# Kernel optimization log

Hardware: AMD Instinct MI355X
Metric: run time of the kernel (lower is better)

The kernel has to match this reference:

```python
import jax, jax.numpy as jnp
import numpy as np

N_NODES = 100000
N_EDGES = 3200000
F_IN = 256
H = 256
L = 256
BN_EPS = 1e-5


def gcn_conv(x, src, dst, deg_inv_sqrt, W, b):
    # x: [N, Fin]; src/dst: [E+N] (self-loops appended); returns [N, Fout]
    h = x @ W  # dense transform first (Fout may be < Fin)
    norm = deg_inv_sqrt[src] * deg_inv_sqrt[dst]  # [E+N]
    msg = h[src] * norm[:, None]                  # gather
    out = jax.ops.segment_sum(msg, dst, num_segments=N_NODES)  # scatter-add
    return out + b


def batch_norm(x, gamma, beta):
    # BatchNorm1d in training mode: per-feature mean/var over the node dim
    mean = jnp.mean(x, axis=0)
    var = jnp.var(x, axis=0)
    return (x - mean) * jax.lax.rsqrt(var + BN_EPS) * gamma + beta


def setup_inputs() -> dict:
    key = jax.random.key(0)
    ks = jax.random.split(key, 8)
    x = jax.random.normal(ks[0], (N_NODES, F_IN), dtype=jnp.float32)
    edge_index = jax.random.randint(ks[1], (2, N_EDGES), 0, N_NODES, dtype=jnp.int64)
    # glorot-ish init for weights
    W1 = jax.random.normal(ks[2], (F_IN, H), dtype=jnp.float32) * (1.0 / np.sqrt(F_IN))
    b1 = jnp.zeros((H,), dtype=jnp.float32)
    W_mu = jax.random.normal(ks[3], (H, L), dtype=jnp.float32) * (1.0 / np.sqrt(H))
    b_mu = jnp.zeros((L,), dtype=jnp.float32)
    W_ls = jax.random.normal(ks[4], (H, L), dtype=jnp.float32) * (1.0 / np.sqrt(H))
    b_ls = jnp.zeros((L,), dtype=jnp.float32)
    gamma = jnp.ones((H,), dtype=jnp.float32)
    beta = jnp.zeros((H,), dtype=jnp.float32)
    return {"x": x, "edge_index": edge_index, "W1": W1, "b1": b1,
            "W_mu": W_mu, "b_mu": b_mu, "W_ls": W_ls, "b_ls": b_ls,
            "gamma": gamma, "beta": beta}


def reference(x, edge_index, W1, b1, W_mu, b_mu, W_ls, b_ls, gamma, beta):
    # Add self-loops once (shared across the three GCNConv layers)
    loop = jnp.arange(N_NODES, dtype=edge_index.dtype)
    src = jnp.concatenate([edge_index[0], loop])
    dst = jnp.concatenate([edge_index[1], loop])
    deg = jax.ops.segment_sum(jnp.ones_like(dst, dtype=jnp.float32), dst,
                              num_segments=N_NODES)
    deg_inv_sqrt = jnp.where(deg > 0, jax.lax.rsqrt(jnp.maximum(deg, 1.0)), 0.0)

    h = gcn_conv(x, src, dst, deg_inv_sqrt, W1, b1)
    h = jax.nn.relu(batch_norm(h, gamma, beta))
    mu = gcn_conv(h, src, dst, deg_inv_sqrt, W_mu, b_mu)
    logstd = gcn_conv(h, src, dst, deg_inv_sqrt, W_ls, b_ls)
    return (mu, logstd)
```

## Files before the change

kernel.cpp:

```cpp
#include <hip/hip_runtime.h>
#include <hip/hip_bf16.h>

#define FEAT 256
#define NPB 512
#define NPB_SHIFT 9
#define MAXBINS 256
#define CAP 20480
#define BIN_CHUNK 8192

typedef __attribute__((ext_vector_type(8))) short bf16x8;
typedef __attribute__((ext_vector_type(8))) ushort u16x8;
typedef __attribute__((ext_vector_type(4))) float f32x4;

__device__ __forceinline__ float bf2f(ushort h) {
    union { unsigned u; float f; } v; v.u = ((unsigned)h) << 16; return v.f;
}
__device__ __forceinline__ ushort f2bf(float f) {
    union { float f; unsigned u; } v; v.f = f;
    unsigned u = v.u;
    return (ushort)((u + 0x7FFFu + ((u >> 16) & 1u)) >> 16);
}


__global__ __launch_bounds__(256) void k_bin(const int* __restrict__ ei, int E, int N,
                                             int* __restrict__ bincur,
                                             int2* __restrict__ binbuf, int nbins) {
    __shared__ int hist[MAXBINS];
    __shared__ int base[MAXBINS];
    int t = threadIdx.x;
    int T = E + N;
    int start = blockIdx.x * BIN_CHUNK;
    int end = min(start + BIN_CHUNK, T);
    for (int b = t; b < nbins; b += 256) hist[b] = 0;
    __syncthreads();
    for (int idx = start + t; idx < end; idx += 256) {
        int d = (idx < E) ? ei[E + idx] : idx - E;
        atomicAdd(&hist[d >> NPB_SHIFT], 1);
    }
    __syncthreads();
    for (int b = t; b < nbins; b += 256) {
        int c = hist[b];
        base[b] = c ? (b * CAP + atomicAdd(&bincur[b], c)) : 0;
        hist[b] = 0;
    }
    __syncthreads();
    for (int idx = start + t; idx < end; idx += 256) {
        int s, d;
        if (idx < E) { s = ei[idx]; d = ei[E + idx]; }
        else         { s = idx - E; d = idx - E; }
        int b = d >> NPB_SHIFT;
        int local = atomicAdd(&hist[b], 1);
        binbuf[base[b] + local] = make_int2(s, d);
    }
}


__global__ __launch_bounds__(512) void k_histcsr(const int2* __restrict__ binbuf,
                                                 const int* __restrict__ bincur,
                                                 int* __restrict__ offs,
                                                 float* __restrict__ dis,
                                                 int* __restrict__ csr, int N, int nbins) {
    __shared__ int bsh[256];
    __shared__ int h[NPB];
    __shared__ int cur[NPB];
    int b = blockIdx.x;
    int t = threadIdx.x;
    int node0 = b * NPB;
    int nn = min(NPB, N - node0);
    if (t < 256) bsh[t] = (t < nbins) ? bincur[t] : 0;
    h[t] = 0; cur[t] = 0;
    __syncthreads();
    for (int d = 1; d < 256; d <<= 1) {
        int x = (t < 256 && t >= d) ? bsh[t - d] : 0;
        __syncthreads();
        if (t < 256) bsh[t] += x;
        __syncthreads();
    }
    int cnt = bincur[b];
    int bpre = bsh[b] - cnt;
    if (b == 0 && t == 0) offs[N] = bsh[nbins - 1];
    int base = b * CAP;
    for (int i = t; i < cnt; i += 512) {
        atomicAdd(&h[binbuf[base + i].y - node0], 1);
    }
    __syncthreads();
    int v = h[t];
    for (int d = 1; d < 512; d <<= 1) {
        int x = (t >= d) ? h[t - d] : 0;
        __syncthreads();
        h[t] += x;
        __syncthreads();
    }
    int myoff = bpre + h[t] - v;
    if (t < nn) {
        offs[node0 + t] = myoff;
        dis[node0 + t] = rsqrtf((float)v);
    }
    h[t] = myoff;
    __syncthreads();
    for (int i = t; i < cnt; i += 512) {
        int2 e = binbuf[base + i];
        int ld = e.y - node0;
        int c = atomicAdd(&cur[ld], 1);
        csr[h[ld] + c] = e.x;
    }
}


__global__ __launch_bounds__(256) void k_cvt(const float* __restrict__ x,
                                             ushort* __restrict__ y,
                                             const float* __restrict__ dis, int n4) {
    int i = blockIdx.x * blockDim.x + threadIdx.x;
    int stride = gridDim.x * blockDim.x;
    for (; i < n4; i += stride) {
        float d = dis[i >> 6];
        float4 v = ((const float4*)x)[i];
        ushort4 o;
        o.x = f2bf(v.x * d); o.y = f2bf(v.y * d);
        o.z = f2bf(v.z * d); o.w = f2bf(v.w * d);
        ((ushort4*)y)[i] = o;
    }
}


__global__ void k_wprep(const float* __restrict__ W1, const float* __restrict__ Wmu,
                        const float* __restrict__ Wls, const float* __restrict__ bmu,
                        const float* __restrict__ bls,
                        ushort* __restrict__ Wt1, ushort* __restrict__ Wtc,
                        float* __restrict__ biasc, float* __restrict__ bnacc) {
    int i = blockIdx.x * 256 + threadIdx.x;
    int m = i >> 16;
    int j = i & 65535;
    int n = j >> 8, k = j & 255;
    const float* W = (m == 0) ? W1 : (m == 1) ? Wmu : Wls;
    ushort v = f2bf(W[k * 256 + n]);
    if (m == 0) Wt1[j] = v;
    else if (m == 1) Wtc[j] = v;
    else Wtc[65536 + j] = v;
    if (i < 512) { biasc[i] = (i < 256) ? bmu[i] : bls[i - 256]; bnacc[i] = 0.f; }
}


__global__ __launch_bounds__(256) void k_agg(const ushort* __restrict__ in,
                                             ushort* __restrict__ out,
                                             const int* __restrict__ offs,
                                             const int* __restrict__ csr,
                                             const float* __restrict__ dis, int N) {
    int wid = blockIdx.x * 4 + ((int)threadIdx.x >> 6);
    if (wid >= N) return;
    int lane = threadIdx.x & 63;
    int half = lane >> 5;
    int l32 = lane & 31;
    int beg = offs[wid], end = offs[wid + 1];
    float acc[8] = {};
    int k = beg;
    for (; k + 16 <= end; k += 16) {
        int s0 = csr[k + half];
        int s1 = csr[k + 2 + half];
        int s2 = csr[k + 4 + half];
        int s3 = csr[k + 6 + half];
        int s4 = csr[k + 8 + half];
        int s5 = csr[k + 10 + half];
        int s6 = csr[k + 12 + half];
        int s7 = csr[k + 14 + half];
        bf16x8 v0 = *(const bf16x8*)(in + (size_t)s0 * FEAT + l32 * 8);
        bf16x8 v1 = *(const bf16x8*)(in + (size_t)s1 * FEAT + l32 * 8);
        bf16x8 v2 = *(const bf16x8*)(in + (size_t)s2 * FEAT + l32 * 8);
        bf16x8 v3 = *(const bf16x8*)(in + (size_t)s3 * FEAT + l32 * 8);
        bf16x8 v4 = *(const bf16x8*)(in + (size_t)s4 * FEAT + l32 * 8);
        bf16x8 v5 = *(const bf16x8*)(in + (size_t)s5 * FEAT + l32 * 8);
        bf16x8 v6 = *(const bf16x8*)(in + (size_t)s6 * FEAT + l32 * 8);
        bf16x8 v7 = *(const bf16x8*)(in + (size_t)s7 * FEAT + l32 * 8);
        #pragma unroll
        for (int j = 0; j < 8; ++j) {
            float t0 = bf2f((ushort)v0[j]) + bf2f((ushort)v1[j]);
            float t1 = bf2f((ushort)v2[j]) + bf2f((ushort)v3[j]);
            float t2 = bf2f((ushort)v4[j]) + bf2f((ushort)v5[j]);
            float t3 = bf2f((ushort)v6[j]) + bf2f((ushort)v7[j]);
            acc[j] += (t0 + t1) + (t2 + t3);
        }
    }
    for (; k + 2 <= end; k += 2) {
        int s = csr[k + half];
        bf16x8 v = *(const bf16x8*)(in + (size_t)s * FEAT + l32 * 8);
        #pragma unroll
        for (int j = 0; j < 8; ++j) acc[j] += bf2f((ushort)v[j]);
    }
    if (k < end && half == 0) {
        int s = csr[k];
        bf16x8 v = *(const bf16x8*)(in + (size_t)s * FEAT + l32 * 8);
        #pragma unroll
        for (int j = 0; j < 8; ++j) acc[j] += bf2f((ushort)v[j]);
    }
    #pragma unroll
    for (int j = 0; j < 8; ++j) acc[j] += __shfl_xor(acc[j], 32, 64);
    if (half == 0) {
        float d = dis[wid];
        u16x8 o;
        #pragma unroll
        for (int j = 0; j < 8; ++j) o[j] = f2bf(acc[j] * d);
        *(u16x8*)(out + (size_t)wid * FEAT + l32 * 8) = o;
    }
}


template <int NCOL, bool BF16OUT>
__global__ __launch_bounds__(256) void k_gemm(const ushort* __restrict__ A,
                                              const ushort* __restrict__ Bt,
                                              const float* __restrict__ bias,
                                              float* __restrict__ C0,
                                              float* __restrict__ C1,
                                              ushort* __restrict__ Cb,
                                              float* __restrict__ bnacc,
                                              int M, int split) {
    __shared__ ushort At[128 * 256];
    __shared__ ushort Bs[128 * 64];
    int t = threadIdx.x;
    int lane = t & 63;
    int wave = t >> 6;
    int wr = wave >> 1, wc = wave & 1;
    int by = blockIdx.x;
    int lo = lane & 15, g = lane >> 4;

    #pragma unroll
    for (int i = 0; i < 16; ++i) {
        int idx = t + i * 256;
        int r = idx >> 5;
        int c = idx & 31;
        int gr = by * 128 + r;
        bf16x8 av = {};
        if (gr < M) av = *(const bf16x8*)(A + (size_t)gr * 256 + c * 8);
        int pc = (c & 24) | ((c & 7) ^ (r & 7));
        *(bf16x8*)(At + r * 256 + pc * 8) = av;
    }
    __syncthreads();

    constexpr int NH = NCOL / 128;
    for (int nh = 0; nh < NH; ++nh) {
        f32x4 acc[4][4] = {};
        for (int kt = 0; kt < 4; ++kt) {
            #pragma unroll
            for (int u = 0; u < 4; ++u) {
                int idx = t + u * 256;
                int r = idx >> 3, c = idx & 7;
                int lc = c ^ (r & 7);
                bf16x8 bv = *(const bf16x8*)(Bt + (size_t)(nh * 128 + r) * 256 + kt * 64 + lc * 8);
                *(bf16x8*)(Bs + r * 64 + c * 8) = bv;
            }
            __syncthreads();
            #pragma unroll
            for (int h = 0; h < 2; ++h) {
                bf16x8 af[4], bfr[4];
                #pragma unroll
                for (int m = 0; m < 4; ++m) {
                    int r = wr * 64 + m * 16 + lo;
                    af[m] = *(const bf16x8*)(At + r * 256 + (kt * 8 + ((h * 4 + g) ^ (r & 7))) * 8);
                }
                #pragma unroll
                for (int n = 0; n < 4; ++n) {
                    int r = wc * 64 + n * 16 + lo;
                    bfr[n] = *(const bf16x8*)(Bs + r * 64 + ((h * 4 + g) ^ (r & 7)) * 8);
                }
                #pragma unroll
                for (int m = 0; m < 4; ++m)
                    #pragma unroll
                    for (int n = 0; n < 4; ++n)
                        acc[m][n] = __builtin_amdgcn_mfma_f32_16x16x32_bf16(
                            af[m], bfr[n], acc[m][n], 0, 0, 0);
            }
            __syncthreads();
        }
        #pragma unroll
        for (int n = 0; n < 4; ++n) {
            int gc = nh * 128 + wc * 64 + n * 16 + lo;
            float bb = bias[gc];
            float s = 0.f, q = 0.f;
            #pragma unroll
            for (int m = 0; m < 4; ++m) {
                f32x4 v = acc[m][n];
                #pragma unroll
                for (int r4 = 0; r4 < 4; ++r4) {
                    int grow = by * 128 + wr * 64 + m * 16 + g * 4 + r4;
                    if (grow < M) {
                        float val = v[r4] + bb;
                        if (BF16OUT) {
                            Cb[(size_t)grow * 256 + gc] = f2bf(val);
                            s += val; q += val * val;
                        } else {
                            float* Cp = C0; int cc = gc;
                            if (gc >= split) { Cp = C1; cc = gc - split; }
                            __builtin_nontemporal_store(val, &Cp[(size_t)grow * 256 + cc]);
                        }
                    }
                }
            }
            if (BF16OUT) {
                s += __shfl_xor(s, 16, 64); s += __shfl_xor(s, 32, 64);
                q += __shfl_xor(q, 16, 64); q += __shfl_xor(q, 32, 64);
                if (g == 0) {
                    atomicAdd(&bnacc[gc], s);
                    atomicAdd(&bnacc[256 + gc], q);
                }
            }
        }
    }
}


__global__ __launch_bounds__(256) void k_bnapply(const ushort* __restrict__ h,
                                                 ushort* __restrict__ o,
                                                 const float* __restrict__ acc,
                                                 const float* __restrict__ gamma,
                                                 const float* __restrict__ beta,
                                                 const float* __restrict__ dis, int Nn) {
    int c4 = (threadIdx.x & 63) * 4;
    int rof = (int)threadIdx.x >> 6;
    float inv = 1.0f / (float)Nn;
    float g[4], b[4];
    #pragma unroll
    for (int j = 0; j < 4; ++j) {
        float mean = acc[c4 + j] * inv;
        float var = acc[FEAT + c4 + j] * inv - mean * mean;
        float rs = rsqrtf(var + 1e-5f);
        g[j] = gamma[c4 + j] * rs;
        b[j] = beta[c4 + j] - mean * g[j];
    }
    for (int r = blockIdx.x * 4 + rof; r < Nn; r += gridDim.x * 4) {
        float d = dis[r];
        ushort4 v = *(const ushort4*)(h + (size_t)r * FEAT + c4);
        float o0 = bf2f(v.x) * g[0] + b[0], o1 = bf2f(v.y) * g[1] + b[1];
        float o2 = bf2f(v.z) * g[2] + b[2], o3 = bf2f(v.w) * g[3] + b[3];
        ushort4 ov;
        ov.x = f2bf((o0 > 0.f ? o0 : 0.f) * d);
        ov.y = f2bf((o1 > 0.f ? o1 : 0.f) * d);
        ov.z = f2bf((o2 > 0.f ? o2 : 0.f) * d);
        ov.w = f2bf((o3 > 0.f ? o3 : 0.f) * d);
        *(ushort4*)(o + (size_t)r * FEAT + c4) = ov;
    }
}


extern "C" void kernel_launch(void* const* d_in, const int* in_sizes, int n_in,
                              void* d_out, int out_size, void* d_ws, size_t ws_size,
                              hipStream_t stream) {
    const float* x     = (const float*)d_in[0];
    const int*   ei    = (const int*)d_in[1];
    const float* W1    = (const float*)d_in[2];
    const float* b1    = (const float*)d_in[3];
    const float* Wmu   = (const float*)d_in[4];
    const float* bmu   = (const float*)d_in[5];
    const float* Wls   = (const float*)d_in[6];
    const float* bls   = (const float*)d_in[7];
    const float* gamma = (const float*)d_in[8];
    const float* beta  = (const float*)d_in[9];

    int N = in_sizes[0] / FEAT;
    int E = in_sizes[1] / 2;
    int nbins = (N + NPB - 1) / NPB;
    int T = E + N;

    float* out = (float*)d_out;
    float* mu  = out;
    float* ls  = out + (size_t)N * FEAT;
    ushort* xtab = (ushort*)mu;
    ushort* H1b  = (ushort*)ls;

    char* p = (char*)d_ws;
    auto alloc = [&](size_t bytes) -> void* {
        void* r = (void*)p;
        p += (bytes + 255) & ~(size_t)255;
        return r;
    };
    ushort* Abuf  = (ushort*)alloc((size_t)N * FEAT * 2);
    int2*   binbuf= (int2*)  alloc((size_t)nbins * CAP * 8);
    int*    csr   = (int*)   alloc((size_t)T * 4);
    int*    offs  = (int*)   alloc((size_t)(N + 1) * 4);
    float*  dis   = (float*) alloc((size_t)N * 4);
    float*  bnacc = (float*) alloc(512 * 4);
    ushort* Wt1   = (ushort*)alloc(65536 * 2);
    ushort* Wtc   = (ushort*)alloc(131072 * 2);
    float*  biasc = (float*) alloc(512 * 4);
    int*    bincur= (int*)   alloc((size_t)nbins * 4);

    hipMemsetAsync(bincur, 0, (size_t)nbins * 4, stream);
    k_bin<<<(T + BIN_CHUNK - 1) / BIN_CHUNK, 256, 0, stream>>>(ei, E, N, bincur, binbuf, nbins);

    k_histcsr<<<nbins, 512, 0, stream>>>(binbuf, bincur, offs, dis, csr, N, nbins);

    k_wprep<<<768, 256, 0, stream>>>(W1, Wmu, Wls, bmu, bls, Wt1, Wtc, biasc, bnacc);
    k_cvt<<<2048, 256, 0, stream>>>(x, xtab, dis, N * FEAT / 4);

    int gblocks = (N + 127) / 128;

    k_agg<<<(N + 3) / 4, 256, 0, stream>>>(xtab, Abuf, offs, csr, dis, N);

    k_gemm<256, true><<<gblocks, 256, 0, stream>>>(Abuf, Wt1, b1, nullptr, nullptr, H1b, bnacc, N, 256);

    k_bnapply<<<2048, 256, 0, stream>>>(H1b, xtab, bnacc, gamma, beta, dis, N);

    k_agg<<<(N + 3) / 4, 256, 0, stream>>>(xtab, Abuf, offs, csr, dis, N);

    k_gemm<512, false><<<gblocks, 256, 0, stream>>>(Abuf, Wtc, biasc, mu, ls, nullptr, nullptr, N, 256);
}
```

Before: 773.9 us.

## Retile GEMM to 128x256 tiles with 8 waves and 2D grid

The GEMM previously staged a full 128x256 A row-block in shared memory and looped over 128-column output halves with 4 waves. Now each 512-thread block computes a 128x256 output tile, streaming both A and B in 64-wide K slices, and the column halves of the second GEMM go to separate blocks on a 2D grid. This cuts shared memory per block and doubles waves per block, aiming for better occupancy and parallelism. The cost is that the second GEMM now loads each A row-block twice.

```diff
diff --git a/kernel.cpp b/kernel.cpp
--- a/kernel.cpp
+++ b/kernel.cpp
@@ -205,102 +205,98 @@
 
 
 template <int NCOL, bool BF16OUT>
-__global__ __launch_bounds__(256) void k_gemm(const ushort* __restrict__ A,
+__global__ __launch_bounds__(512) void k_gemm(const ushort* __restrict__ A,
                                               const ushort* __restrict__ Bt,
                                               const float* __restrict__ bias,
                                               float* __restrict__ C0,
                                               float* __restrict__ C1,
                                               ushort* __restrict__ Cb,
                                               float* __restrict__ bnacc,
-                                              int M, int split) {
-    __shared__ ushort At[128 * 256];
-    __shared__ ushort Bs[128 * 64];
+                                              int M) {
+    __shared__ ushort As[128 * 64];
+    __shared__ ushort Bs[256 * 64];
     int t = threadIdx.x;
     int lane = t & 63;
     int wave = t >> 6;
-    int wr = wave >> 1, wc = wave & 1;
-    int by = blockIdx.x;
+    int wr = wave >> 2, wc = wave & 3;
+    int bx = blockIdx.x, by = blockIdx.y;
     int lo = lane & 15, g = lane >> 4;
-
-    #pragma unroll
-    for (int i = 0; i < 16; ++i) {
-        int idx = t + i * 256;
-        int r = idx >> 5;
-        int c = idx & 31;
-        int gr = by * 128 + r;
-        bf16x8 av = {};
-        if (gr < M) av = *(const bf16x8*)(A + (size_t)gr * 256 + c * 8);
-        int pc = (c & 24) | ((c & 7) ^ (r & 7));
-        *(bf16x8*)(At + r * 256 + pc * 8) = av;
-    }
-    __syncthreads();
-
-    constexpr int NH = NCOL / 128;
-    for (int nh = 0; nh < NH; ++nh) {
-        f32x4 acc[4][4] = {};
-        for (int kt = 0; kt < 4; ++kt) {
-            #pragma unroll
-            for (int u = 0; u < 4; ++u) {
-                int idx = t + u * 256;
-                int r = idx >> 3, c = idx & 7;
-                int lc = c ^ (r & 7);
-                bf16x8 bv = *(const bf16x8*)(Bt + (size_t)(nh * 128 + r) * 256 + kt * 64 + lc * 8);
-                *(bf16x8*)(Bs + r * 64 + c * 8) = bv;
-            }
-            __syncthreads();
-            #pragma unroll
-            for (int h = 0; h < 2; ++h) {
-                bf16x8 af[4], bfr[4];
-                #pragma unroll
-                for (int m = 0; m < 4; ++m) {
-                    int r = wr * 64 + m * 16 + lo;
-                    af[m] = *(const bf16x8*)(At + r * 256 + (kt * 8 + ((h * 4 + g) ^ (r & 7))) * 8);
-                }
-                #pragma unroll
-                for (int n = 0; n < 4; ++n) {
-                    int r = wc * 64 + n * 16 + lo;
-                    bfr[n] = *(const bf16x8*)(Bs + r * 64 + ((h * 4 + g) ^ (r & 7)) * 8);
-                }
-                #pragma unroll
-                for (int m = 0; m < 4; ++m)
-                    #pragma unroll
-                    for (int n = 0; n < 4; ++n)
-                        acc[m][n] = __builtin_amdgcn_mfma_f32_16x16x32_bf16(
-                            af[m], bfr[n], acc[m][n], 0, 0, 0);
-            }
-            __syncthreads();
-        }
-        #pragma unroll
-        for (int n = 0; n < 4; ++n) {
-            int gc = nh * 128 + wc * 64 + n * 16 + lo;
-            float bb = bias[gc];
-            float s = 0.f, q = 0.f;
+    f32x4 acc[4][4] = {};
+    int chunk = t & 7;
+    int row8 = t >> 3;
+
+    for (int kt = 0; kt < 4; ++kt) {
+        int k0 = kt * 64;
+        #pragma unroll
+        for (int i = 0; i < 2; ++i) {
+            int r = row8 + i * 64;
+            int lc = chunk ^ (r & 7);
+            int gr = by * 128 + r;
+            bf16x8 av = {};
+            if (gr < M) av = *(const bf16x8*)(A + (size_t)gr * 256 + k0 + lc * 8);
+            *(bf16x8*)(As + r * 64 + chunk * 8) = av;
+        }
+        #pragma unroll
+        for (int i = 0; i < 4; ++i) {
+            int r = row8 + i * 64;
+            int lc = chunk ^ (r & 7);
+            int gn = bx * 256 + r;
+            bf16x8 bv = *(const bf16x8*)(Bt + (size_t)gn * 256 + k0 + lc * 8);
+            *(bf16x8*)(Bs + r * 64 + chunk * 8) = bv;
+        }
+        __syncthreads();
+        #pragma unroll
+        for (int h = 0; h < 2; ++h) {
+            bf16x8 af[4], bfr[4];
             #pragma unroll
             for (int m = 0; m < 4; ++m) {
-                f32x4 v = acc[m][n];
+                int r = wr * 64 + m * 16 + lo;
+                af[m] = *(const bf16x8*)(As + r * 64 + (((h * 4 + g) ^ (r & 7)) * 8));
+            }
+            #pragma unroll
+            for (int n = 0; n < 4; ++n) {
+                int r = wc * 64 + n * 16 + lo;
+                bfr[n] = *(const bf16x8*)(Bs + r * 64 + (((h * 4 + g) ^ (r & 7)) * 8));
+            }
+            #pragma unroll
+            for (int m = 0; m < 4; ++m)
                 #pragma unroll
-                for (int r4 = 0; r4 < 4; ++r4) {
-                    int grow = by * 128 + wr * 64 + m * 16 + g * 4 + r4;
-                    if (grow < M) {
-                        float val = v[r4] + bb;
-                        if (BF16OUT) {
-                            Cb[(size_t)grow * 256 + gc] = f2bf(val);
-                            s += val; q += val * val;
-                        } else {
-                            float* Cp = C0; int cc = gc;
-                            if (gc >= split) { Cp = C1; cc = gc - split; }
-                            __builtin_nontemporal_store(val, &Cp[(size_t)grow * 256 + cc]);
-                        }
+                for (int n = 0; n < 4; ++n)
+                    acc[m][n] = __builtin_amdgcn_mfma_f32_16x16x32_bf16(
+                        af[m], bfr[n], acc[m][n], 0, 0, 0);
+        }
+        __syncthreads();
+    }
+    #pragma unroll
+    for (int n = 0; n < 4; ++n) {
+        int gc = bx * 256 + wc * 64 + n * 16 + lo;
+        float bb = bias[gc];
+        float s = 0.f, q = 0.f;
+        #pragma unroll
+        for (int m = 0; m < 4; ++m) {
+            f32x4 v = acc[m][n];
+            #pragma unroll
+            for (int r4 = 0; r4 < 4; ++r4) {
+                int grow = by * 128 + wr * 64 + m * 16 + g * 4 + r4;
+                if (grow < M) {
+                    float val = v[r4] + bb;
+                    if (BF16OUT) {
+                        Cb[(size_t)grow * 256 + gc] = f2bf(val);
+                        s += val; q += val * val;
+                    } else {
+                        float* Cp = C0; int cc = gc;
+                        if (gc >= 256) { Cp = C1; cc = gc - 256; }
+                        __builtin_nontemporal_store(val, &Cp[(size_t)grow * 256 + cc]);
                     }
                 }
             }
-            if (BF16OUT) {
-                s += __shfl_xor(s, 16, 64); s += __shfl_xor(s, 32, 64);
-                q += __shfl_xor(q, 16, 64); q += __shfl_xor(q, 32, 64);
-                if (g == 0) {
-                    atomicAdd(&bnacc[gc], s);
-                    atomicAdd(&bnacc[256 + gc], q);
-                }
+        }
+        if (BF16OUT) {
+            s += __shfl_xor(s, 16, 64); s += __shfl_xor(s, 32, 64);
+            q += __shfl_xor(q, 16, 64); q += __shfl_xor(q, 32, 64);
+            if (g == 0) {
+                atomicAdd(&bnacc[gc], s);
+                atomicAdd(&bnacc[256 + gc], q);
             }
         }
     }
@@ -394,11 +390,13 @@
 
     k_agg<<<(N + 3) / 4, 256, 0, stream>>>(xtab, Abuf, offs, csr, dis, N);
 
-    k_gemm<256, true><<<gblocks, 256, 0, stream>>>(Abuf, Wt1, b1, nullptr, nullptr, H1b, bnacc, N, 256);
+    dim3 g1(1, gblocks);
+    k_gemm<256, true><<<g1, 512, 0, stream>>>(Abuf, Wt1, b1, nullptr, nullptr, H1b, bnacc, N);
 
     k_bnapply<<<2048, 256, 0, stream>>>(H1b, xtab, bnacc, gamma, beta, dis, N);
 
     k_agg<<<(N + 3) / 4, 256, 0, stream>>>(xtab, Abuf, offs, csr, dis, N);
 
-    k_gemm<512, false><<<gblocks, 256, 0, stream>>>(Abuf, Wtc, biasc, mu, ls, nullptr, nullptr, N, 256);
-}
+    dim3 g2(2, gblocks);
+    k_gemm<512, false><<<g2, 512, 0, stream>>>(Abuf, Wtc, biasc, mu, ls, nullptr, nullptr, N);
+}
```

New measurement: 748.1 us. 3.3% less time.
